# Kernel optimization log

Measured on AMD Instinct MI355X. Metric: run time of the kernel, lower is better.

Reference implementation:

```python
import jax, jax.numpy as jnp
import numpy as np

H = 2048        # hidden_dim
D = 128         # head_dim
NQ = H // D     # 16 query heads
NKV = 4         # kv heads (GQA)
ROTARY_BASE = 10000.0


def _rope_cos_sin(seq_len, dim, dtype):
    inv_freq = 1.0 / (ROTARY_BASE ** (jnp.arange(0, dim, 2, dtype=jnp.float32) / dim))
    t = jnp.arange(seq_len, dtype=jnp.float32)
    freqs = jnp.outer(t, inv_freq)          # [S, D/2]
    return jnp.cos(freqs).astype(dtype), jnp.sin(freqs).astype(dtype)


def _apply_rope(x, cos, sin):
    # x: [B, S, H, D], non-interleaved (rotate-half) convention of flash-attn
    d2 = x.shape[-1] // 2
    x1, x2 = x[..., :d2], x[..., d2:]
    c = cos[None, :, None, :]
    s = sin[None, :, None, :]
    return jnp.concatenate([x1 * c - x2 * s, x2 * c + x1 * s], axis=-1)


def setup_inputs() -> dict:
    key = jax.random.key(0)
    ks = jax.random.split(key, 9)
    B, S = 2, 2048
    sd = 1.0 / np.sqrt(H)
    return {
        "hidden_states": jax.random.normal(ks[0], (B, S, H), jnp.float32),
        "Wq": jax.random.normal(ks[1], (H, NQ * D), jnp.float32) * sd,
        "bq": jnp.zeros((NQ * D,), jnp.float32),
        "Wk": jax.random.normal(ks[2], (H, NKV * D), jnp.float32) * sd,
        "bk": jnp.zeros((NKV * D,), jnp.float32),
        "Wv": jax.random.normal(ks[3], (H, NKV * D), jnp.float32) * sd,
        "bv": jnp.zeros((NKV * D,), jnp.float32),
        "Wc": jax.random.normal(ks[4], (NQ * D, H), jnp.float32) * sd,
        "bc": jnp.zeros((H,), jnp.float32),
    }


def reference(hidden_states, Wq, bq, Wk, bk, Wv, bv, Wc, bc):
    B, S, _ = hidden_states.shape
    scale = 1.0 / np.sqrt(D)  # scale_attn_by_inverse_layer_idx=False

    q = (hidden_states @ Wq + bq).reshape(B, S, NQ, D)
    k = (hidden_states @ Wk + bk).reshape(B, S, NKV, D)
    v = (hidden_states @ Wv + bv).reshape(B, S, NKV, D)

    cos, sin = _rope_cos_sin(S, D, q.dtype)
    q = _apply_rope(q, cos, sin)
    k = _apply_rope(k, cos, sin)

    # GQA: expand kv heads to match query heads
    rep = NQ // NKV
    k_e = jnp.repeat(k, rep, axis=2)  # [B, S, NQ, D]
    v_e = jnp.repeat(v, rep, axis=2)

    scores = jnp.einsum("bshd,bthd->bhst", q, k_e) * scale  # [B, NQ, S, S]
    causal = jnp.tril(jnp.ones((S, S), bool))
    scores = jnp.where(causal[None, None], scores, jnp.finfo(scores.dtype).min)
    probs = jax.nn.softmax(scores, axis=-1)
    attn = jnp.einsum("bhst,bthd->bshd", probs, v_e)  # [B, S, NQ, D]

    out = attn.reshape(B, S, NQ * D) @ Wc + bc  # resid dropout p=0 (eval)
    return out, k, v
```

## Files before the change

### kernel.cpp

```cpp
#include <hip/hip_runtime.h>
#include <math.h>

typedef unsigned short u16;
typedef __attribute__((ext_vector_type(8))) short s16x8;
typedef __attribute__((ext_vector_type(4))) float f32x4;
typedef __attribute__((ext_vector_type(16))) float f32x16;
typedef unsigned u32x2u __attribute__((ext_vector_type(2)));

#define B_  2
#define S_  2048
#define H_  2048
#define D_  128
#define NQ_ 16
#define NKV_ 4
#define M_  (B_*S_)
#define NQKV_ 3072

#define MFMA16(a,b,c) __builtin_amdgcn_mfma_f32_16x16x32_bf16(a,b,c,0,0,0)
#define MFMA32(a,b,c) __builtin_amdgcn_mfma_f32_32x32x16_bf16(a,b,c,0,0,0)

__device__ __forceinline__ u16 f2bf(float x) {
  union { float f; unsigned u; } v; v.f = x;
  unsigned r = v.u + 0x7fffu + ((v.u >> 16) & 1u);
  return (u16)(r >> 16);
}
__device__ __forceinline__ float bf2f(u16 x) {
  union { unsigned u; float f; } v; v.u = ((unsigned)x) << 16;
  return v.f;
}

__device__ __forceinline__ unsigned cvtpk(float lo, float hi) {
  unsigned r;
  asm("v_cvt_pk_bf16_f32 %0, %1, %2" : "=v"(r) : "v"(lo), "v"(hi));
  return r;
}

__device__ __forceinline__ void plswap(unsigned &x, unsigned &y) {
#if __has_builtin(__builtin_amdgcn_permlane32_swap)
  u32x2u r = __builtin_amdgcn_permlane32_swap(x, y, false, false);
  x = r[0]; y = r[1];
#else
  const bool hb = (threadIdx.x & 32) != 0;
  unsigned ex = (unsigned)__shfl_xor((int)x, 32, 64);
  unsigned ey = (unsigned)__shfl_xor((int)y, 32, 64);
  unsigned nx = hb ? ey : x;
  unsigned ny = hb ? y : ex;
  x = nx; y = ny;
#endif
}

__global__ __launch_bounds__(256) void cvt_x(const float* __restrict__ X, u16* __restrict__ Xb, long n4) {
  const f32x4* X4 = (const f32x4*)X;
  for (long i = (long)blockIdx.x*256 + threadIdx.x; i < n4; i += (long)gridDim.x*256) {
    f32x4 v = X4[i];
    union { u16 u[4]; unsigned long long ll; } p;
    p.u[0] = f2bf(v[0]); p.u[1] = f2bf(v[1]); p.u[2] = f2bf(v[2]); p.u[3] = f2bf(v[3]);
    ((unsigned long long*)Xb)[i] = p.ll;
  }
}

__global__ __launch_bounds__(256) void wtrans(const float* __restrict__ W, u16* __restrict__ Wt,
                                              int N, int K) {
  __shared__ float t[32][33];
  const int n0 = blockIdx.x*32, k0 = blockIdx.y*32;
  const int tx = threadIdx.x, ty = threadIdx.y;
  #pragma unroll
  for (int i = 0; i < 32; i += 8) t[ty+i][tx] = W[(long)(k0+ty+i)*N + n0 + tx];
  __syncthreads();
  #pragma unroll
  for (int i = 0; i < 32; i += 8) Wt[(long)(n0+ty+i)*K + k0 + tx] = f2bf(t[tx][ty+i]);
}

__global__ __launch_bounds__(256) void vtrans(const u16* __restrict__ QKV, u16* __restrict__ Vt) {
  __shared__ u16 t[32][33];
  const int bk = blockIdx.z;
  const int s0 = blockIdx.x*32, d0 = blockIdx.y*32;
  const int tx = threadIdx.x, ty = threadIdx.y;
  const int b = bk >> 2, kvh = bk & 3;
  #pragma unroll
  for (int i = 0; i < 32; i += 8)
    t[ty+i][tx] = QKV[(long)(b*S_ + s0+ty+i)*NQKV_ + 2560 + kvh*128 + d0 + tx];
  __syncthreads();
  #pragma unroll
  for (int i = 0; i < 32; i += 8)
    Vt[((long)bk*D_ + d0+ty+i)*S_ + s0 + tx] = t[tx][ty+i];
}

__global__ void concat_bias(const float* bq, const float* bk, const float* bv, float* bqkv) {
  int i = blockIdx.x*256 + threadIdx.x;
  if (i < NQKV_)
    bqkv[i] = (i < 2048) ? bq[i] : ((i < 2560) ? bk[i-2048] : bv[i-2560]);
}

__global__ void rope_tab(float* __restrict__ cosb, float* __restrict__ sinb) {
  int i = blockIdx.x*256 + threadIdx.x;
  int t = i >> 6, d = i & 63;
  float inv = powf(10000.0f, -((float)(2*d)) * (1.0f/128.0f));
  float fr = (float)t * inv;
  float sv, cv;
  sincosf(fr, &sv, &cv);
  cosb[i] = cv; sinb[i] = sv;
}

__global__ __launch_bounds__(256) void rope_qkv(
    const u16* __restrict__ QKV, const float* __restrict__ cosb, const float* __restrict__ sinb,
    u16* __restrict__ Qb, u16* __restrict__ Kb,
    float* __restrict__ kout, float* __restrict__ vout)
{
  const float QS = 0.08838834764831845f * 1.4426950408889634f;
  const int m = blockIdx.x;
  const int b = m >> 11, s = m & 2047;
  const int tid = threadIdx.x;
  const u16* row = QKV + (long)m * NQKV_;
  const int d = tid & 63;
  const float c  = cosb[s*64 + d];
  const float sn = sinb[s*64 + d];
  #pragma unroll
  for (int i = 0; i < 4; i++) {
    int hh = (tid + i*256) >> 6;
    float x1 = bf2f(row[hh*128 + d]), x2 = bf2f(row[hh*128 + d + 64]);
    float o1 = x1*c - x2*sn, o2 = x2*c + x1*sn;
    long base = ((long)(b*NQ_ + hh)*S_ + s)*D_;
    Qb[base + d] = f2bf(o1*QS);
    Qb[base + d + 64] = f2bf(o2*QS);
  }
  {
    int kh = tid >> 6;
    float x1 = bf2f(row[2048 + kh*128 + d]), x2 = bf2f(row[2048 + kh*128 + d + 64]);
    float o1 = x1*c - x2*sn, o2 = x2*c + x1*sn;
    long kb = ((long)(b*NKV_ + kh)*S_ + s)*D_;
    Kb[kb + d] = f2bf(o1);
    Kb[kb + d + 64] = f2bf(o2);
    long ko = ((long)m*NKV_ + kh)*D_;
    kout[ko + d] = o1;
    kout[ko + d + 64] = o2;
  }
  #pragma unroll
  for (int i = 0; i < 2; i++) {
    int e = tid + i*256;
    vout[(long)m*512 + e] = bf2f(row[2560 + e]);
  }
}

template<int BN, typename OutT>
__global__ __launch_bounds__(512, 2) void gemm256(
    const u16* __restrict__ A, const u16* __restrict__ Bm,
    const float* __restrict__ bias, OutT* __restrict__ C,
    int M, int N, int K)
{
  __shared__ u16 As[2][256*64];
  __shared__ u16 Bs[2][BN*64];
  constexpr int WCc = (BN == 256) ? 4 : 2;
  constexpr int MI  = (BN == 256) ? 8 : 4;
  constexpr int LB  = BN/64;
  constexpr int TOT = 4 + LB;

  const int tid = threadIdx.x;
  const int lane = tid & 63, w = tid >> 6;
  const int r16 = lane & 15, g = lane >> 4;
  const int wrn = w / WCc, wcn = w % WCc;
  const int abase = wrn * (MI*16);
  const int bbase = wcn * 64;

  const int gx = gridDim.x;
  const int nwg = gx * gridDim.y;
  const int id = blockIdx.y * gx + blockIdx.x;
  const int cpx = nwg >> 3;
  const int sid = (id & 7) * cpx + (id >> 3);
  const long m0 = (long)(sid / gx) * 256;
  const long n0 = (long)(sid % gx) * BN;

  const u16* Ag = A + m0 * K;
  const u16* Bg = Bm + n0 * K;

  auto stage = [&](int buf, int k0) {
    #pragma unroll
    for (int i = 0; i < 4; i++) {
      const int slot = i*512 + tid;
      const int row = slot >> 3, cg = slot & 7;
      const u16* src = Ag + (long)row*K + k0 + ((cg ^ (row & 7)) * 8);
      __builtin_amdgcn_global_load_lds(
          (const __attribute__((address_space(1))) unsigned int*)src,
          (__attribute__((address_space(3))) unsigned int*)&As[buf][slot*8], 16, 0, 0);
    }
    #pragma unroll
    for (int i = 0; i < LB; i++) {
      const int slot = i*512 + tid;
      const int row = slot >> 3, cg = slot & 7;
      const u16* src = Bg + (long)row*K + k0 + ((cg ^ (row & 7)) * 8);
      __builtin_amdgcn_global_load_lds(
          (const __attribute__((address_space(1))) unsigned int*)src,
          (__attribute__((address_space(3))) unsigned int*)&Bs[buf][slot*8], 16, 0, 0);
    }
  };

  f32x4 acc[MI][4] = {};
  const int nt = K >> 6;

  stage(0, 0);
  stage(1, 64);
  for (int t = 0; t < nt; t++) {
    if (t + 1 < nt) {
      if constexpr (TOT == 8) asm volatile("s_waitcnt vmcnt(8)" ::: "memory");
      else                    asm volatile("s_waitcnt vmcnt(6)" ::: "memory");
    } else {
      asm volatile("s_waitcnt vmcnt(0)" ::: "memory");
    }
    __builtin_amdgcn_s_barrier();

    const u16* as = &As[t & 1][0];
    const u16* bs = &Bs[t & 1][0];
    #pragma unroll
    for (int k = 0; k < 2; k++) {
      s16x8 bfr[4];
      #pragma unroll
      for (int nj = 0; nj < 4; nj++) {
        const int R = bbase + nj*16 + r16;
        bfr[nj] = *(const s16x8*)&bs[R*64 + (((k*4 + g) ^ (R & 7)) * 8)];
      }
      __builtin_amdgcn_s_setprio(1);
      #pragma unroll
      for (int mi = 0; mi < MI; mi++) {
        const int R = abase + mi*16 + r16;
        s16x8 afr = *(const s16x8*)&as[R*64 + (((k*4 + g) ^ (R & 7)) * 8)];
        #pragma unroll
        for (int nj = 0; nj < 4; nj++)
          acc[mi][nj] = MFMA16(afr, bfr[nj], acc[mi][nj]);
      }
      __builtin_amdgcn_s_setprio(0);
    }
    __builtin_amdgcn_s_barrier();
    if (t + 2 < nt) stage(t & 1, (t + 2) << 6);
  }

  #pragma unroll
  for (int mi = 0; mi < MI; mi++) {
    #pragma unroll
    for (int nj = 0; nj < 4; nj++) {
      const int col = bbase + nj*16 + r16;
      const float bv = bias[n0 + col];
      #pragma unroll
      for (int r = 0; r < 4; r++) {
        const long row = m0 + abase + mi*16 + g*4 + r;
        if constexpr (sizeof(OutT) == 2)
          C[row * N + n0 + col] = (OutT)f2bf(acc[mi][nj][r] + bv);
        else
          C[row * N + n0 + col] = (OutT)(acc[mi][nj][r] + bv);
      }
    }
  }
}

__global__ __launch_bounds__(256, 2) void attn_kernel(
    const u16* __restrict__ Qb, const u16* __restrict__ Kb,
    const u16* __restrict__ Vt, u16* __restrict__ Ob)
{
  __shared__ u16 Ks[2][64*128];
  __shared__ u16 Vs[2][64*128];
  const int tid = threadIdx.x;
  const int lane = tid & 63, w = tid >> 6;
  const int l31 = lane & 31, hi = lane >> 5;
  const int id = blockIdx.x;
  const int bh = id & 31;
  const int b = bh >> 4, h = bh & 15;
  const int p = id >> 5;
  const int qt = (p < 8) ? (15 - p) : (p - 8);
  const int kvh = h >> 2;
  const int q0w = qt*128 + w*32;
  const int nt = 2*qt + 2;

  const u16* Qg = Qb + (((long)(b*NQ_ + h))*S_ + q0w)*D_;
  const u16* Kg = Kb + ((long)(b*NKV_ + kvh))*S_*D_;
  const u16* Vg = Vt + ((long)(b*NKV_ + kvh))*D_*S_;

  s16x8 qf[8];
  #pragma unroll
  for (int ks = 0; ks < 8; ks++)
    qf[ks] = *(const s16x8*)&Qg[l31*D_ + ks*16 + hi*8];

  f32x16 po[4] = {};
  float mrow = -1e30f, lrow = 0.f;

  auto stage = [&](int buf, int kv0s) {
    #pragma unroll
    for (int i = 0; i < 4; i++) {
      const int c = i*4 + w;
      const int G = c*64 + lane;
      const int krow = G >> 4, kcg = G & 15;
      const u16* gk = Kg + (long)(kv0s + krow)*D_ + ((kcg ^ (krow & 15)) * 8);
      __builtin_amdgcn_global_load_lds(
          (const __attribute__((address_space(1))) unsigned int*)gk,
          (__attribute__((address_space(3))) unsigned int*)&Ks[buf][c*512], 16, 0, 0);
      const int o = c*512 + lane*8;
      const int d2 = o >> 7, t16 = (o >> 3) & 15;
      const int gidx = t16 ^ (d2 & 15);
      const int dsr = ((gidx >> 3) << 6) + d2;
      const u16* gv = Vg + (long)dsr*S_ + kv0s + ((gidx & 7) * 8);
      __builtin_amdgcn_global_load_lds(
          (const __attribute__((address_space(1))) unsigned int*)gv,
          (__attribute__((address_space(3))) unsigned int*)&Vs[buf][c*512], 16, 0, 0);
    }
  };

  auto compute = [&](int buf, int t) {
    const int kv0 = t*64;
    if (kv0 > q0w + 31) return;
    f32x16 sc[2] = {};
    __builtin_amdgcn_s_setprio(1);
    #pragma unroll
    for (int ks = 0; ks < 8; ks++) {
      #pragma unroll
      for (int ct = 0; ct < 2; ct++) {
        const int row = ct*32 + l31;
        s16x8 kf = *(const s16x8*)&Ks[buf][row*128 + ((ks*16 + hi*8) ^ ((row & 15)*8))];
        sc[ct] = MFMA32(kf, qf[ks], sc[ct]);
      }
    }
    __builtin_amdgcn_s_setprio(0);
    if (kv0 + 63 > q0w) {
      const int qrow = q0w + l31;
      #pragma unroll
      for (int ct = 0; ct < 2; ct++)
        #pragma unroll
        for (int r = 0; r < 16; r++) {
          int kv = kv0 + ct*32 + (r & 3) + 8*(r >> 2) + 4*hi;
          if (kv > qrow) sc[ct][r] = -3.0e38f;
        }
    }
    float pm = sc[0][0];
    #pragma unroll
    for (int ct = 0; ct < 2; ct++)
      #pragma unroll
      for (int r = 0; r < 16; r++) pm = fmaxf(pm, sc[ct][r]);
    pm = fmaxf(pm, __shfl_xor(pm, 32, 64));
    if (!__all(pm - mrow <= 8.0f)) {
      float mn = fmaxf(mrow, pm);
      float fr = exp2f(mrow - mn);
      mrow = mn;
      lrow *= fr;
      #pragma unroll
      for (int r = 0; r < 16; r++) {
        float frv = __shfl(fr, (r & 3) + 8*(r >> 2) + 4*hi, 64);
        #pragma unroll
        for (int dt = 0; dt < 4; dt++) po[dt][r] *= frv;
      }
    }
    float ps = 0.f;
    #pragma unroll
    for (int ct = 0; ct < 2; ct++)
      #pragma unroll
      for (int r = 0; r < 16; r++) {
        float pv = exp2f(sc[ct][r] - mrow);
        sc[ct][r] = pv;
        ps += pv;
      }
    ps += __shfl_xor(ps, 32, 64);
    lrow += ps;
    unsigned mw[2][8];
    #pragma unroll
    for (int ct = 0; ct < 2; ct++)
      #pragma unroll
      for (int wd = 0; wd < 8; wd++)
        mw[ct][wd] = cvtpk(sc[ct][2*wd], sc[ct][2*wd + 1]);
    s16x8 pa[4];
    #pragma unroll
    for (int ct = 0; ct < 2; ct++)
      #pragma unroll
      for (int pp = 0; pp < 2; pp++) {
        unsigned a0 = mw[ct][4*pp + 0], b0 = mw[ct][4*pp + 2];
        unsigned a1 = mw[ct][4*pp + 1], b1 = mw[ct][4*pp + 3];
        plswap(a0, b0);
        plswap(a1, b1);
        union { unsigned u[4]; s16x8 v; } pu;
        pu.u[0] = a0; pu.u[1] = a1; pu.u[2] = b0; pu.u[3] = b1;
        pa[ct*2 + pp] = pu.v;
      }
    __builtin_amdgcn_s_setprio(1);
    #pragma unroll
    for (int ks2 = 0; ks2 < 4; ks2++)
      #pragma unroll
      for (int dt = 0; dt < 4; dt++) {
        const int d = dt*32 + l31, d2 = d & 63;
        const int gidx = ((d >> 6) << 3) + ks2*2 + hi;
        s16x8 vf = *(const s16x8*)&Vs[buf][d2*128 + ((gidx ^ (d2 & 15)) * 8)];
        po[dt] = MFMA32(pa[ks2], vf, po[dt]);
      }
    __builtin_amdgcn_s_setprio(0);
  };

  stage(0, 0);
  for (int t = 0; t < nt; t += 2) {
    stage(1, (t + 1)*64);
    asm volatile("s_waitcnt vmcnt(8)" ::: "memory");
    __builtin_amdgcn_s_barrier();
    compute(0, t);
    __builtin_amdgcn_s_barrier();
    if (t + 2 < nt) {
      stage(0, (t + 2)*64);
      asm volatile("s_waitcnt vmcnt(8)" ::: "memory");
    } else {
      asm volatile("s_waitcnt vmcnt(0)" ::: "memory");
    }
    __builtin_amdgcn_s_barrier();
    compute(1, t + 1);
    __builtin_amdgcn_s_barrier();
  }

  float inv = 1.0f / lrow;
  #pragma unroll
  for (int r = 0; r < 16; r++) {
    const int qr = (r & 3) + 8*(r >> 2) + 4*hi;
    float invq = __shfl(inv, qr, 64);
    const long q = (long)q0w + qr;
    #pragma unroll
    for (int dt = 0; dt < 4; dt++)
      Ob[((long)b*S_ + q)*H_ + h*D_ + dt*32 + l31] = f2bf(po[dt][r]*invq);
  }
}

extern "C" void kernel_launch(void* const* d_in, const int* in_sizes, int n_in,
                              void* d_out, int out_size, void* d_ws, size_t ws_size,
                              hipStream_t stream) {
  const float* hs = (const float*)d_in[0];
  const float* Wq = (const float*)d_in[1];
  const float* bq = (const float*)d_in[2];
  const float* Wk = (const float*)d_in[3];
  const float* bk = (const float*)d_in[4];
  const float* Wv = (const float*)d_in[5];
  const float* bv = (const float*)d_in[6];
  const float* Wc = (const float*)d_in[7];
  const float* bc = (const float*)d_in[8];

  float* out  = (float*)d_out;
  float* kout = out + (long)M_*H_;
  float* vout = kout + (long)M_*NKV_*D_;

  char* ws = (char*)d_ws;
  u16*  Xbf   = (u16*)ws;
  u16*  Wqkvt = Xbf + (long)M_*H_;
  u16*  Wct   = Wqkvt + (long)NQKV_*H_;
  float* bqkv = (float*)(Wct + (long)H_*H_);
  u16*  QKV   = (u16*)(bqkv + NQKV_);
  float* cosb = (float*)(QKV + (long)M_*NQKV_);
  float* sinb = cosb + S_*64;
  u16*  Qbf   = (u16*)(sinb + S_*64);
  u16*  Kbf   = Qbf + (long)B_*NQ_*S_*D_;
  u16*  Vtb   = Kbf + (long)B_*NKV_*S_*D_;
  u16*  Obf   = Vtb + (long)B_*NKV_*D_*S_;

  cvt_x<<<2048, 256, 0, stream>>>(hs, Xbf, (long)M_*H_/4);
  wtrans<<<dim3(64,64), dim3(32,8), 0, stream>>>(Wq, Wqkvt, 2048, 2048);
  wtrans<<<dim3(16,64), dim3(32,8), 0, stream>>>(Wk, Wqkvt + 2048L*2048, 512, 2048);
  wtrans<<<dim3(16,64), dim3(32,8), 0, stream>>>(Wv, Wqkvt + 2560L*2048, 512, 2048);
  wtrans<<<dim3(64,64), dim3(32,8), 0, stream>>>(Wc, Wct, 2048, 2048);
  concat_bias<<<12, 256, 0, stream>>>(bq, bk, bv, bqkv);
  rope_tab<<<512, 256, 0, stream>>>(cosb, sinb);

  gemm256<256, u16><<<dim3(NQKV_/256, M_/256), 512, 0, stream>>>(
      Xbf, Wqkvt, bqkv, QKV, M_, NQKV_, H_);
  rope_qkv<<<M_, 256, 0, stream>>>(QKV, cosb, sinb, Qbf, Kbf, kout, vout);
  vtrans<<<dim3(S_/32, D_/32, B_*NKV_), dim3(32,8), 0, stream>>>(QKV, Vtb);
  attn_kernel<<<dim3(512), 256, 0, stream>>>(Qbf, Kbf, Vtb, Obf);
  gemm256<128, float><<<dim3(H_/128, M_/256), 512, 0, stream>>>(
      Obf, Wct, bc, out, M_, H_, H_);
}
```

Baseline: 221.8 us.

## Restructure GEMM into four-phase ping-pong schedule with split half-tile loads

Replaces the GEMM main loop with a four-phase schedule. Each K-step is split into quadrant sub-tiles (A half × B half), and prefetches of the next tiles' halves are interleaved between phases, with barriers around each MFMA cluster. The goal is better overlap of global-to-LDS loads and LDS reads with MFMA work, and fewer stalls than the single wait-then-compute loop. The cost is more barriers per iteration and tricky vmcnt accounting, which risks stalls or hazards if the counts are off.

```diff
diff --git a/kernel.cpp b/kernel.cpp
--- a/kernel.cpp
+++ b/kernel.cpp
@@ -47,6 +47,12 @@
   unsigned ny = hb ? y : ex;
   x = nx; y = ny;
 #endif
+}
+
+__device__ __forceinline__ void gload_lds16(const u16* src, u16* dst) {
+  __builtin_amdgcn_global_load_lds(
+      (const __attribute__((address_space(1))) unsigned int*)src,
+      (__attribute__((address_space(3))) unsigned int*)dst, 16, 0, 0);
 }
 
 __global__ __launch_bounds__(256) void cvt_x(const float* __restrict__ X, u16* __restrict__ Xb, long n4) {
@@ -143,24 +149,25 @@
 }
 
 template<int BN, typename OutT>
-__global__ __launch_bounds__(512, 2) void gemm256(
+__global__ __launch_bounds__(512, 2) void gemm8p(
     const u16* __restrict__ A, const u16* __restrict__ Bm,
     const float* __restrict__ bias, OutT* __restrict__ C,
     int M, int N, int K)
 {
+  constexpr int WN  = (BN == 256) ? 4 : 2;
+  constexpr int WM  = 8 / WN;
+  constexpr int JA  = 8 / WM;
+  constexpr int JB  = 2;
+  constexpr int RW  = 128 / WM;
+  constexpr int CW  = (BN/2) / WN;
+  constexpr int MI2 = 2*JA;
   __shared__ u16 As[2][256*64];
   __shared__ u16 Bs[2][BN*64];
-  constexpr int WCc = (BN == 256) ? 4 : 2;
-  constexpr int MI  = (BN == 256) ? 8 : 4;
-  constexpr int LB  = BN/64;
-  constexpr int TOT = 4 + LB;
 
   const int tid = threadIdx.x;
   const int lane = tid & 63, w = tid >> 6;
   const int r16 = lane & 15, g = lane >> 4;
-  const int wrn = w / WCc, wcn = w % WCc;
-  const int abase = wrn * (MI*16);
-  const int bbase = wcn * 64;
+  const int wrn = w / WN, wcn = w % WN;
 
   const int gx = gridDim.x;
   const int nwg = gx * gridDim.y;
@@ -173,82 +180,99 @@
   const u16* Ag = A + m0 * K;
   const u16* Bg = Bm + n0 * K;
 
-  auto stage = [&](int buf, int k0) {
-    #pragma unroll
-    for (int i = 0; i < 4; i++) {
+  auto stageA = [&](int buf, int h, int k0) {
+    #pragma unroll
+    for (int i = 0; i < 2; i++) {
       const int slot = i*512 + tid;
-      const int row = slot >> 3, cg = slot & 7;
+      const int row = h*128 + (slot >> 3), cg = slot & 7;
       const u16* src = Ag + (long)row*K + k0 + ((cg ^ (row & 7)) * 8);
-      __builtin_amdgcn_global_load_lds(
-          (const __attribute__((address_space(1))) unsigned int*)src,
-          (__attribute__((address_space(3))) unsigned int*)&As[buf][slot*8], 16, 0, 0);
-    }
-    #pragma unroll
-    for (int i = 0; i < LB; i++) {
+      gload_lds16(src, &As[buf][h*8192 + slot*8]);
+    }
+  };
+  auto stageB = [&](int buf, int h, int k0) {
+    #pragma unroll
+    for (int i = 0; i < BN/128; i++) {
       const int slot = i*512 + tid;
-      const int row = slot >> 3, cg = slot & 7;
+      const int row = h*(BN/2) + (slot >> 3), cg = slot & 7;
       const u16* src = Bg + (long)row*K + k0 + ((cg ^ (row & 7)) * 8);
-      __builtin_amdgcn_global_load_lds(
-          (const __attribute__((address_space(1))) unsigned int*)src,
-          (__attribute__((address_space(3))) unsigned int*)&Bs[buf][slot*8], 16, 0, 0);
+      gload_lds16(src, &Bs[buf][h*(BN*32) + slot*8]);
     }
   };
 
-  f32x4 acc[MI][4] = {};
+  f32x4 acc[MI2][4] = {};
+  s16x8 Ar[JA][2], Br[JB][2];
   const int nt = K >> 6;
 
-  stage(0, 0);
-  stage(1, 64);
+#define PHASE(BUF, MH, NH, RDA, RDB, STMT)                                        \
+  do {                                                                            \
+    if (RDA) {                                                                    \
+      _Pragma("unroll") for (int j = 0; j < JA; j++)                              \
+        _Pragma("unroll") for (int kk = 0; kk < 2; kk++) {                        \
+          const int R = (MH)*128 + wrn*RW + j*16 + r16;                           \
+          Ar[j][kk] = *(const s16x8*)&As[BUF][R*64 + (((kk*4 + g) ^ (R & 7))*8)]; \
+        }                                                                         \
+    }                                                                             \
+    if (RDB) {                                                                    \
+      _Pragma("unroll") for (int jj = 0; jj < JB; jj++)                           \
+        _Pragma("unroll") for (int kk = 0; kk < 2; kk++) {                        \
+          const int Cc = (NH)*(BN/2) + wcn*CW + jj*16 + r16;                      \
+          Br[jj][kk] = *(const s16x8*)&Bs[BUF][Cc*64 + (((kk*4 + g) ^ (Cc & 7))*8)]; \
+        }                                                                         \
+    }                                                                             \
+    STMT;                                                                         \
+    __builtin_amdgcn_s_barrier();                                                 \
+    asm volatile("s_waitcnt lgkmcnt(0)" ::: "memory");                            \
+    __builtin_amdgcn_sched_barrier(0);                                            \
+    __builtin_amdgcn_s_setprio(1);                                                \
+    _Pragma("unroll") for (int j = 0; j < JA; j++)                                \
+      _Pragma("unroll") for (int jj = 0; jj < JB; jj++)                           \
+        _Pragma("unroll") for (int kk = 0; kk < 2; kk++)                          \
+          acc[(MH)*JA + j][(NH)*JB + jj] =                                        \
+            MFMA16(Ar[j][kk], Br[jj][kk], acc[(MH)*JA + j][(NH)*JB + jj]);        \
+    __builtin_amdgcn_s_setprio(0);                                                \
+    __builtin_amdgcn_s_barrier();                                                 \
+  } while (0)
+
+  stageA(0, 0, 0); stageA(0, 1, 0); stageB(0, 0, 0); stageB(0, 1, 0);
+  if (nt > 1) { stageA(1, 0, 64); stageB(1, 1, 64); }
+
   for (int t = 0; t < nt; t++) {
-    if (t + 1 < nt) {
-      if constexpr (TOT == 8) asm volatile("s_waitcnt vmcnt(8)" ::: "memory");
-      else                    asm volatile("s_waitcnt vmcnt(6)" ::: "memory");
+    const int X = t & 1, Y = X ^ 1;
+    if (t == nt - 1) {
+      asm volatile("s_waitcnt vmcnt(0)" ::: "memory");
+    } else if constexpr (BN == 256) {
+      asm volatile("s_waitcnt vmcnt(4)" ::: "memory");
     } else {
-      asm volatile("s_waitcnt vmcnt(0)" ::: "memory");
+      asm volatile("s_waitcnt vmcnt(3)" ::: "memory");
     }
     __builtin_amdgcn_s_barrier();
-
-    const u16* as = &As[t & 1][0];
-    const u16* bs = &Bs[t & 1][0];
-    #pragma unroll
-    for (int k = 0; k < 2; k++) {
-      s16x8 bfr[4];
-      #pragma unroll
-      for (int nj = 0; nj < 4; nj++) {
-        const int R = bbase + nj*16 + r16;
-        bfr[nj] = *(const s16x8*)&bs[R*64 + (((k*4 + g) ^ (R & 7)) * 8)];
-      }
-      __builtin_amdgcn_s_setprio(1);
-      #pragma unroll
-      for (int mi = 0; mi < MI; mi++) {
-        const int R = abase + mi*16 + r16;
-        s16x8 afr = *(const s16x8*)&as[R*64 + (((k*4 + g) ^ (R & 7)) * 8)];
+    PHASE(X, 0, 0, true,  true,  { if (t+1 < nt) stageA(Y, 1, (t+1)*64); });
+    PHASE(X, 0, 1, false, true,  { if (t+1 < nt) stageB(Y, 0, (t+1)*64); });
+    PHASE(X, 1, 1, true,  false, { if (t+2 < nt) stageA(X, 0, (t+2)*64); });
+    PHASE(X, 1, 0, false, true,  { if (t+2 < nt) stageB(X, 1, (t+2)*64); });
+  }
+#undef PHASE
+
+  #pragma unroll
+  for (int mh = 0; mh < 2; mh++)
+    #pragma unroll
+    for (int j = 0; j < JA; j++)
+      #pragma unroll
+      for (int nh = 0; nh < 2; nh++)
         #pragma unroll
-        for (int nj = 0; nj < 4; nj++)
-          acc[mi][nj] = MFMA16(afr, bfr[nj], acc[mi][nj]);
-      }
-      __builtin_amdgcn_s_setprio(0);
-    }
-    __builtin_amdgcn_s_barrier();
-    if (t + 2 < nt) stage(t & 1, (t + 2) << 6);
-  }
-
-  #pragma unroll
-  for (int mi = 0; mi < MI; mi++) {
-    #pragma unroll
-    for (int nj = 0; nj < 4; nj++) {
-      const int col = bbase + nj*16 + r16;
-      const float bv = bias[n0 + col];
-      #pragma unroll
-      for (int r = 0; r < 4; r++) {
-        const long row = m0 + abase + mi*16 + g*4 + r;
-        if constexpr (sizeof(OutT) == 2)
-          C[row * N + n0 + col] = (OutT)f2bf(acc[mi][nj][r] + bv);
-        else
-          C[row * N + n0 + col] = (OutT)(acc[mi][nj][r] + bv);
-      }
-    }
-  }
+        for (int jj = 0; jj < JB; jj++) {
+          const int col = nh*(BN/2) + wcn*CW + jj*16 + r16;
+          const float bv = bias[n0 + col];
+          #pragma unroll
+          for (int r = 0; r < 4; r++) {
+            const long row = m0 + mh*128 + wrn*RW + j*16 + g*4 + r;
+            const float vv = acc[mh*JA + j][nh*JB + jj][r] + bv;
+            if constexpr (sizeof(OutT) == 2)
+              C[row * N + n0 + col] = (OutT)f2bf(vv);
+            else
+              C[row * N + n0 + col] = (OutT)vv;
+          }
+        }
 }
 
 __global__ __launch_bounds__(256, 2) void attn_kernel(
@@ -288,17 +312,13 @@
       const int G = c*64 + lane;
       const int krow = G >> 4, kcg = G & 15;
       const u16* gk = Kg + (long)(kv0s + krow)*D_ + ((kcg ^ (krow & 15)) * 8);
-      __builtin_amdgcn_global_load_lds(
-          (const __attribute__((address_space(1))) unsigned int*)gk,
-          (__attribute__((address_space(3))) unsigned int*)&Ks[buf][c*512], 16, 0, 0);
+      gload_lds16(gk, &Ks[buf][c*512]);
       const int o = c*512 + lane*8;
       const int d2 = o >> 7, t16 = (o >> 3) & 15;
       const int gidx = t16 ^ (d2 & 15);
       const int dsr = ((gidx >> 3) << 6) + d2;
       const u16* gv = Vg + (long)dsr*S_ + kv0s + ((gidx & 7) * 8);
-      __builtin_amdgcn_global_load_lds(
-          (const __attribute__((address_space(1))) unsigned int*)gv,
-          (__attribute__((address_space(3))) unsigned int*)&Vs[buf][c*512], 16, 0, 0);
+      gload_lds16(gv, &Vs[buf][c*512]);
     }
   };
 
@@ -456,11 +476,11 @@
   concat_bias<<<12, 256, 0, stream>>>(bq, bk, bv, bqkv);
   rope_tab<<<512, 256, 0, stream>>>(cosb, sinb);
 
-  gemm256<256, u16><<<dim3(NQKV_/256, M_/256), 512, 0, stream>>>(
+  gemm8p<256, u16><<<dim3(NQKV_/256, M_/256), 512, 0, stream>>>(
       Xbf, Wqkvt, bqkv, QKV, M_, NQKV_, H_);
   rope_qkv<<<M_, 256, 0, stream>>>(QKV, cosb, sinb, Qbf, Kbf, kout, vout);
   vtrans<<<dim3(S_/32, D_/32, B_*NKV_), dim3(32,8), 0, stream>>>(QKV, Vtb);
   attn_kernel<<<dim3(512), 256, 0, stream>>>(Qbf, Kbf, Vtb, Obf);
-  gemm256<128, float><<<dim3(H_/128, M_/256), 512, 0, stream>>>(
+  gemm8p<128, float><<<dim3(H_/128, M_/256), 512, 0, stream>>>(
       Obf, Wct, bc, out, M_, H_, H_);
 }
```

After: 214.5 us. -3.3%, faster.
